# Performance work log

Measured on AMD Instinct MI355X. Metric: run time of the kernel, lower is better.

The kernel has to match this reference:

```python
import jax, jax.numpy as jnp
import numpy as np

HIDDEN = 2048
INTER = 8192
COMPRESSION = 128.9

def _n_ctrl(out_size, in_size):
    return max(16, int(out_size * in_size / COMPRESSION))

def _catmull_rom_grid(n_ctrl, n_samples):
    # static (numpy, float64) sampling grid over [0, n_ctrl-1] to avoid fp32 precision loss
    t = np.linspace(0.0, n_ctrl - 1.0, n_samples, dtype=np.float64)
    i = np.clip(np.floor(t).astype(np.int64), 0, n_ctrl - 2)
    f = (t - i).astype(np.float32)
    idx = np.stack([np.clip(i + k, 0, n_ctrl - 1) for k in (-1, 0, 1, 2)], axis=0)  # [4, N]
    return jnp.asarray(idx.astype(np.int32)), jnp.asarray(f)

def spline_reconstruct(control_points, out_size, in_size):
    """Cubic (Catmull-Rom, order-3) interpolation of 1D control points to a dense [out,in] weight."""
    n = out_size * in_size
    idx, f = _catmull_rom_grid(control_points.shape[0], n)
    p0, p1, p2, p3 = control_points[idx[0]], control_points[idx[1]], control_points[idx[2]], control_points[idx[3]]
    f2 = f * f
    f3 = f2 * f
    w = 0.5 * (2.0 * p1 + (p2 - p0) * f
               + (2.0 * p0 - 5.0 * p1 + 4.0 * p2 - p3) * f2
               + (3.0 * p1 - p0 - 3.0 * p2 + p3) * f3)
    return w.reshape(out_size, in_size)

def setup_inputs() -> dict:
    key = jax.random.key(0)
    k0, k1, k2, k3 = jax.random.split(key, 4)
    hidden_states = jax.random.normal(k0, (4, 2048, HIDDEN), dtype=jnp.float32)
    gate_cp = jax.random.normal(k1, (_n_ctrl(INTER, HIDDEN),), dtype=jnp.float32) * 0.02
    up_cp = jax.random.normal(k2, (_n_ctrl(INTER, HIDDEN),), dtype=jnp.float32) * 0.02
    down_cp = jax.random.normal(k3, (_n_ctrl(HIDDEN, INTER),), dtype=jnp.float32) * 0.02
    return {"hidden_states": hidden_states, "gate_cp": gate_cp, "up_cp": up_cp, "down_cp": down_cp}

def reference(hidden_states, gate_cp, up_cp, down_cp):
    gate_w = spline_reconstruct(gate_cp, INTER, HIDDEN)   # [I, H]
    up_w = spline_reconstruct(up_cp, INTER, HIDDEN)       # [I, H]
    down_w = spline_reconstruct(down_cp, HIDDEN, INTER)   # [H, I]
    gate = jnp.einsum('bsh,ih->bsi', hidden_states, gate_w)
    up = jnp.einsum('bsh,ih->bsi', hidden_states, up_w)
    inter = jax.nn.silu(gate) * up
    return jnp.einsum('bsi,hi->bsh', inter, down_w)
```

## Files before the change

### kernel.cpp

```cpp
#include <hip/hip_runtime.h>
#include <hip/hip_bf16.h>
#include <math.h>

using bf16 = __hip_bfloat16;
typedef __bf16 bf16x8 __attribute__((ext_vector_type(8)));
typedef float  f32x4  __attribute__((ext_vector_type(4)));

#define BK 64

__global__ void spline_recon8_kernel(const float* __restrict__ cp,
                                     bf16* __restrict__ w,
                                     int n8, int n_ctrl, double step) {
    int k8 = blockIdx.x * blockDim.x + threadIdx.x;
    if (k8 >= n8) return;
    long long kbase = (long long)k8 * 8;
    bf16x8 o;
#pragma unroll
    for (int u = 0; u < 8; ++u) {
        double t = (double)(kbase + u) * step;
        int i = (int)t;
        if (i > n_ctrl - 2) i = n_ctrl - 2;
        float f = (float)(t - (double)i);
        float p0 = cp[i > 0 ? i - 1 : 0];
        float p1 = cp[i];
        float p2 = cp[i + 1];
        float p3 = cp[(i + 2) <= (n_ctrl - 1) ? (i + 2) : (n_ctrl - 1)];
        float f2 = f * f;
        float f3 = f2 * f;
        float v = 0.5f * (2.0f * p1
                          + (p2 - p0) * f
                          + (2.0f * p0 - 5.0f * p1 + 4.0f * p2 - p3) * f2
                          + (3.0f * p1 - p0 - 3.0f * p2 + p3) * f3);
        o[u] = (__bf16)v;
    }
    *reinterpret_cast<bf16x8*>(w + kbase) = o;
}

__global__ void cvt_f32_bf16_8_kernel(const float4* __restrict__ x,
                                      bf16* __restrict__ y, int n8) {
    int k = blockIdx.x * blockDim.x + threadIdx.x;
    if (k >= n8) return;
    float4 a = x[2 * k];
    float4 b = x[2 * k + 1];
    bf16x8 o;
    o[0] = (__bf16)a.x; o[1] = (__bf16)a.y; o[2] = (__bf16)a.z; o[3] = (__bf16)a.w;
    o[4] = (__bf16)b.x; o[5] = (__bf16)b.y; o[6] = (__bf16)b.z; o[7] = (__bf16)b.w;
    *reinterpret_cast<bf16x8*>(y + (long long)k * 8) = o;
}

__device__ __forceinline__ void async_load16(const bf16* g, bf16* l) {
    __builtin_amdgcn_global_load_lds(
        (const __attribute__((address_space(1))) void*)g,
        (__attribute__((address_space(3))) void*)l,
        16, 0, 0);
}

__device__ __forceinline__ void raw_barrier() {
    asm volatile("" ::: "memory");
    __builtin_amdgcn_s_barrier();
    asm volatile("" ::: "memory");
}

#define WAIT_VM6() asm volatile("s_waitcnt vmcnt(6)" ::: "memory")
#define WAIT_VM0() asm volatile("s_waitcnt vmcnt(0)" ::: "memory")

__global__ __launch_bounds__(512, 2) void fused_gate_up_kernel(
    const bf16* __restrict__ A,
    const bf16* __restrict__ Bg,
    const bf16* __restrict__ Bu,
    bf16* __restrict__ C,
    int M, int N, int K) {
    __shared__ __align__(16) bf16 smem[2 * 3 * 128 * BK];
    bf16* As0  = smem;
    bf16* Bgs0 = smem + 8192;
    bf16* Bus0 = smem + 16384;
    bf16* As1  = smem + 24576;
    bf16* Bgs1 = smem + 32768;
    bf16* Bus1 = smem + 40960;

    const int tid  = threadIdx.x;
    const int lane = tid & 63;
    const int wave = tid >> 6;
    const int wq   = wave & 3;
    const int wm   = (wq >> 1) * 64;
    const int wn   = (wq & 1) * 64;
    const bool is_gate = wave < 4;

    const long long brow = (long long)blockIdx.y * 128;
    const long long bcol = (long long)blockIdx.x * 128;

    const int srow = tid >> 3;
    const int skb  = ((tid & 7) ^ (srow & 7)) * 8;
    const bf16* ga0 = A  + (brow + srow) * (long long)K + skb;
    const bf16* ga1 = A  + (brow + srow + 64) * (long long)K + skb;
    const bf16* gg0 = Bg + (bcol + srow) * (long long)K + skb;
    const bf16* gg1 = Bg + (bcol + srow + 64) * (long long)K + skb;
    const bf16* gu0 = Bu + (bcol + srow) * (long long)K + skb;
    const bf16* gu1 = Bu + (bcol + srow + 64) * (long long)K + skb;

    const int fm = wm + (lane & 15);
    const int fn = wn + (lane & 15);
    const int qk = lane >> 4;

    f32x4 acc[4][4] = {};

#define STAGE_F(dA, dG, dU, t)                                             \
    do {                                                                   \
        long long off = (long long)(t) * BK;                               \
        async_load16(ga0 + off, (dA) + tid * 8);                           \
        async_load16(ga1 + off, (dA) + 4096 + tid * 8);                    \
        async_load16(gg0 + off, (dG) + tid * 8);                           \
        async_load16(gg1 + off, (dG) + 4096 + tid * 8);                    \
        async_load16(gu0 + off, (dU) + tid * 8);                           \
        async_load16(gu1 + off, (dU) + 4096 + tid * 8);                    \
    } while (0)

#define COMPUTE_F(sA, sG, sU)                                              \
    do {                                                                   \
        const bf16* sB = is_gate ? (sG) : (sU);                            \
        _Pragma("unroll")                                                  \
        for (int h = 0; h < 2; ++h) {                                      \
            bf16x8 afr[4], bfr[4];                                         \
            const int hc = (h << 2) | qk;                                  \
            const int ccA = (hc ^ (fm & 7)) * 8;                           \
            const int ccB = (hc ^ (fn & 7)) * 8;                           \
            _Pragma("unroll")                                              \
            for (int i = 0; i < 4; ++i)                                    \
                afr[i] = *reinterpret_cast<const bf16x8*>(                 \
                    &(sA)[(fm + i * 16) * BK + ccA]);                      \
            _Pragma("unroll")                                              \
            for (int j = 0; j < 4; ++j)                                    \
                bfr[j] = *reinterpret_cast<const bf16x8*>(                 \
                    &sB[(fn + j * 16) * BK + ccB]);                        \
            _Pragma("unroll")                                              \
            for (int i = 0; i < 4; ++i)                                    \
                _Pragma("unroll")                                          \
                for (int j = 0; j < 4; ++j)                                \
                    acc[i][j] = __builtin_amdgcn_mfma_f32_16x16x32_bf16(   \
                        afr[i], bfr[j], acc[i][j], 0, 0, 0);               \
        }                                                                  \
    } while (0)

    const int nt = K / BK;

    STAGE_F(As0, Bgs0, Bus0, 0);
    STAGE_F(As1, Bgs1, Bus1, 1);
    WAIT_VM6();
    raw_barrier();

    for (int t = 0; t + 2 < nt; t += 2) {
        COMPUTE_F(As0, Bgs0, Bus0);
        raw_barrier();
        STAGE_F(As0, Bgs0, Bus0, t + 2);
        WAIT_VM6();
        raw_barrier();
        COMPUTE_F(As1, Bgs1, Bus1);
        raw_barrier();
        STAGE_F(As1, Bgs1, Bus1, t + 3);
        WAIT_VM6();
        raw_barrier();
    }
    COMPUTE_F(As0, Bgs0, Bus0);
    WAIT_VM0();
    raw_barrier();
    COMPUTE_F(As1, Bgs1, Bus1);
#undef STAGE_F
#undef COMPUTE_F

    bf16* Epi = smem;
    if (is_gate) {
#pragma unroll
        for (int i = 0; i < 4; ++i)
#pragma unroll
            for (int j = 0; j < 4; ++j)
#pragma unroll
                for (int r = 0; r < 4; ++r) {
                    int row = wm + i * 16 + (lane >> 4) * 4 + r;
                    int col = wn + j * 16 + (lane & 15);
                    float v = acc[i][j][r];
                    float s = v / (1.0f + expf(-v));
                    Epi[row * 128 + col] = __float2bfloat16(s);
                }
    }
    __syncthreads();
    if (!is_gate) {
#pragma unroll
        for (int i = 0; i < 4; ++i)
#pragma unroll
            for (int j = 0; j < 4; ++j)
#pragma unroll
                for (int r = 0; r < 4; ++r) {
                    int row = wm + i * 16 + (lane >> 4) * 4 + r;
                    int col = wn + j * 16 + (lane & 15);
                    float s = __bfloat162float(Epi[row * 128 + col]);
                    float v = s * acc[i][j][r];
                    C[(brow + row) * (long long)N + bcol + col] = __float2bfloat16(v);
                }
    }
}

__global__ __launch_bounds__(512, 2) void gemm_down6_kernel(
    const bf16* __restrict__ A,
    const bf16* __restrict__ B,
    float* __restrict__ C,
    int M, int N, int K) {
    __shared__ __align__(16) bf16 smem[2 * 3 * 128 * BK];
    bf16* As0 = smem;
    bf16* Bs0 = smem + 128 * BK;
    bf16* As1 = smem + 3 * 128 * BK;
    bf16* Bs1 = smem + 4 * 128 * BK;

    const int tid  = threadIdx.x;
    const int lane = tid & 63;
    const int wave = tid >> 6;
    const int wm   = (wave >> 2) * 64;
    const int wn   = (wave & 3) * 64;

    const int b = blockIdx.x;
    const long long brow = (long long)((b & 7) * 8 + (b >> 6)) * 128;
    const long long bcol = (long long)((b >> 3) & 7) * 256;

    const int srow = tid >> 3;
    const int skb  = ((tid & 7) ^ (srow & 7)) * 8;
    const bf16* ga0 = A + (brow + srow) * (long long)K + skb;
    const bf16* ga1 = A + (brow + srow + 64) * (long long)K + skb;
    const bf16* gb0 = B + (bcol + srow) * (long long)K + skb;
    const bf16* gb1 = B + (bcol + srow + 64) * (long long)K + skb;
    const bf16* gb2 = B + (bcol + srow + 128) * (long long)K + skb;
    const bf16* gb3 = B + (bcol + srow + 192) * (long long)K + skb;

    const int fm = wm + (lane & 15);
    const int fn = wn + (lane & 15);
    const int qk = lane >> 4;

    f32x4 acc[4][4] = {};

#define STAGE_DOWN(dA, dB, t)                                              \
    do {                                                                   \
        long long off = (long long)(t) * BK;                               \
        async_load16(ga0 + off, (dA) + tid * 8);                           \
        async_load16(ga1 + off, (dA) + 4096 + tid * 8);                    \
        async_load16(gb0 + off, (dB) + tid * 8);                           \
        async_load16(gb1 + off, (dB) + 4096 + tid * 8);                    \
        async_load16(gb2 + off, (dB) + 8192 + tid * 8);                    \
        async_load16(gb3 + off, (dB) + 12288 + tid * 8);                   \
    } while (0)

#define COMPUTE_DOWN(sA, sB)                                               \
    do {                                                                   \
        _Pragma("unroll")                                                  \
        for (int h = 0; h < 2; ++h) {                                      \
            bf16x8 afr[4], bfr[4];                                         \
            const int hc = (h << 2) | qk;                                  \
            const int ccA = (hc ^ (fm & 7)) * 8;                           \
            const int ccB = (hc ^ (fn & 7)) * 8;                           \
            _Pragma("unroll")                                              \
            for (int i = 0; i < 4; ++i)                                    \
                afr[i] = *reinterpret_cast<const bf16x8*>(                 \
                    &(sA)[(fm + i * 16) * BK + ccA]);                      \
            _Pragma("unroll")                                              \
            for (int j = 0; j < 4; ++j)                                    \
                bfr[j] = *reinterpret_cast<const bf16x8*>(                 \
                    &(sB)[(fn + j * 16) * BK + ccB]);                      \
            _Pragma("unroll")                                              \
            for (int i = 0; i < 4; ++i)                                    \
                _Pragma("unroll")                                          \
                for (int j = 0; j < 4; ++j)                                \
                    acc[i][j] = __builtin_amdgcn_mfma_f32_16x16x32_bf16(   \
                        afr[i], bfr[j], acc[i][j], 0, 0, 0);               \
        }                                                                  \
    } while (0)

    const int nt = K / BK;

    STAGE_DOWN(As0, Bs0, 0);
    STAGE_DOWN(As1, Bs1, 1);
    WAIT_VM6();
    raw_barrier();

    for (int t = 0; t + 2 < nt; t += 2) {
        COMPUTE_DOWN(As0, Bs0);
        raw_barrier();
        STAGE_DOWN(As0, Bs0, t + 2);
        WAIT_VM6();
        raw_barrier();
        COMPUTE_DOWN(As1, Bs1);
        raw_barrier();
        STAGE_DOWN(As1, Bs1, t + 3);
        WAIT_VM6();
        raw_barrier();
    }
    COMPUTE_DOWN(As0, Bs0);
    WAIT_VM0();
    raw_barrier();
    COMPUTE_DOWN(As1, Bs1);
#undef STAGE_DOWN
#undef COMPUTE_DOWN

#pragma unroll
    for (int i = 0; i < 4; ++i)
#pragma unroll
        for (int j = 0; j < 4; ++j)
#pragma unroll
            for (int r = 0; r < 4; ++r) {
                long long row = brow + wm + i * 16 + qk * 4 + r;
                long long col = bcol + wn + j * 16 + (lane & 15);
                C[row * N + col] = acc[i][j][r];
            }
}

extern "C" void kernel_launch(void* const* d_in, const int* in_sizes, int n_in,
                              void* d_out, int out_size, void* d_ws, size_t ws_size,
                              hipStream_t stream) {
    const float* hs  = (const float*)d_in[0];
    const float* gcp = (const float*)d_in[1];
    const float* ucp = (const float*)d_in[2];
    const float* dcp = (const float*)d_in[3];

    const int M = 8192;
    const int H = 2048;
    const int I = 8192;
    const int NW = H * I;
    const int n_ctrl_g = in_sizes[1];
    const int n_ctrl_u = in_sizes[2];
    const int n_ctrl_d = in_sizes[3];

    bf16* Xb    = (bf16*)d_ws;
    bf16* Wg    = Xb + (size_t)M * H;
    bf16* Wu    = Wg + (size_t)NW;
    bf16* Wd    = Wu + (size_t)NW;
    bf16* inter = Wd + (size_t)NW;

    const int nX8 = (M * H) / 8;
    cvt_f32_bf16_8_kernel<<<(nX8 + 255) / 256, 256, 0, stream>>>(
        (const float4*)hs, Xb, nX8);

    double step_g = (double)(n_ctrl_g - 1) / (double)(NW - 1);
    double step_u = (double)(n_ctrl_u - 1) / (double)(NW - 1);
    double step_d = (double)(n_ctrl_d - 1) / (double)(NW - 1);
    const int n8 = NW / 8;
    spline_recon8_kernel<<<(n8 + 255) / 256, 256, 0, stream>>>(gcp, Wg, n8, n_ctrl_g, step_g);
    spline_recon8_kernel<<<(n8 + 255) / 256, 256, 0, stream>>>(ucp, Wu, n8, n_ctrl_u, step_u);
    spline_recon8_kernel<<<(n8 + 255) / 256, 256, 0, stream>>>(dcp, Wd, n8, n_ctrl_d, step_d);

    fused_gate_up_kernel<<<dim3(I / 128, M / 128), 512, 0, stream>>>(
        Xb, Wg, Wu, inter, M, I, H);

    gemm_down6_kernel<<<512, 512, 0, stream>>>(
        inter, Wd, (float*)d_out, M, H, I);
}
```

Measured before the change: 952.4 us.

## Enlarge GEMM tiles to 256 rows and compute gate and up per wave

The fused gate/up kernel now uses a 256x128 tile in which every wave computes both the gate and up accumulators. The SiLU*up epilogue happens in registers, so the LDS round-trip and the extra syncthreads go away and the A tile gets more reuse. The down GEMM moves to 256x256 tiles with 8x4 accumulator fragments per wave, halving the grid to 256 blocks. Each wave now holds twice the accumulators and LDS use grows to 128KB per block, so register spills or lower occupancy are possible despite the launch bound of 2.

```diff
diff --git a/kernel.cpp b/kernel.cpp
--- a/kernel.cpp
+++ b/kernel.cpp
@@ -61,38 +61,38 @@
     asm volatile("" ::: "memory");
 }
 
-#define WAIT_VM6() asm volatile("s_waitcnt vmcnt(6)" ::: "memory")
-#define WAIT_VM0() asm volatile("s_waitcnt vmcnt(0)" ::: "memory")
-
-__global__ __launch_bounds__(512, 2) void fused_gate_up_kernel(
+#define WAIT_VM8()  asm volatile("s_waitcnt vmcnt(8)" ::: "memory")
+#define WAIT_VM0()  asm volatile("s_waitcnt vmcnt(0)" ::: "memory")
+
+__global__ __launch_bounds__(512, 2) void fused_gate_up2_kernel(
     const bf16* __restrict__ A,
     const bf16* __restrict__ Bg,
     const bf16* __restrict__ Bu,
     bf16* __restrict__ C,
     int M, int N, int K) {
-    __shared__ __align__(16) bf16 smem[2 * 3 * 128 * BK];
+    __shared__ __align__(16) bf16 smem[2 * 2 * 256 * BK];
     bf16* As0  = smem;
-    bf16* Bgs0 = smem + 8192;
-    bf16* Bus0 = smem + 16384;
-    bf16* As1  = smem + 24576;
-    bf16* Bgs1 = smem + 32768;
-    bf16* Bus1 = smem + 40960;
+    bf16* Bgs0 = smem + 16384;
+    bf16* Bus0 = smem + 24576;
+    bf16* As1  = smem + 32768;
+    bf16* Bgs1 = smem + 49152;
+    bf16* Bus1 = smem + 57344;
 
     const int tid  = threadIdx.x;
     const int lane = tid & 63;
     const int wave = tid >> 6;
-    const int wq   = wave & 3;
-    const int wm   = (wq >> 1) * 64;
-    const int wn   = (wq & 1) * 64;
-    const bool is_gate = wave < 4;
-
-    const long long brow = (long long)blockIdx.y * 128;
+    const int wm   = (wave >> 1) * 64;
+    const int wn   = (wave & 1) * 64;
+
+    const long long brow = (long long)blockIdx.y * 256;
     const long long bcol = (long long)blockIdx.x * 128;
 
     const int srow = tid >> 3;
     const int skb  = ((tid & 7) ^ (srow & 7)) * 8;
     const bf16* ga0 = A  + (brow + srow) * (long long)K + skb;
     const bf16* ga1 = A  + (brow + srow + 64) * (long long)K + skb;
+    const bf16* ga2 = A  + (brow + srow + 128) * (long long)K + skb;
+    const bf16* ga3 = A  + (brow + srow + 192) * (long long)K + skb;
     const bf16* gg0 = Bg + (bcol + srow) * (long long)K + skb;
     const bf16* gg1 = Bg + (bcol + srow + 64) * (long long)K + skb;
     const bf16* gu0 = Bu + (bcol + srow) * (long long)K + skb;
@@ -102,13 +102,16 @@
     const int fn = wn + (lane & 15);
     const int qk = lane >> 4;
 
-    f32x4 acc[4][4] = {};
+    f32x4 acc_g[4][4] = {};
+    f32x4 acc_u[4][4] = {};
 
 #define STAGE_F(dA, dG, dU, t)                                             \
     do {                                                                   \
         long long off = (long long)(t) * BK;                               \
         async_load16(ga0 + off, (dA) + tid * 8);                           \
         async_load16(ga1 + off, (dA) + 4096 + tid * 8);                    \
+        async_load16(ga2 + off, (dA) + 8192 + tid * 8);                    \
+        async_load16(ga3 + off, (dA) + 12288 + tid * 8);                   \
         async_load16(gg0 + off, (dG) + tid * 8);                           \
         async_load16(gg1 + off, (dG) + 4096 + tid * 8);                    \
         async_load16(gu0 + off, (dU) + tid * 8);                           \
@@ -117,10 +120,9 @@
 
 #define COMPUTE_F(sA, sG, sU)                                              \
     do {                                                                   \
-        const bf16* sB = is_gate ? (sG) : (sU);                            \
         _Pragma("unroll")                                                  \
         for (int h = 0; h < 2; ++h) {                                      \
-            bf16x8 afr[4], bfr[4];                                         \
+            bf16x8 afr[4], bgr[4], bur[4];                                 \
             const int hc = (h << 2) | qk;                                  \
             const int ccA = (hc ^ (fm & 7)) * 8;                           \
             const int ccB = (hc ^ (fn & 7)) * 8;                           \
@@ -129,15 +131,21 @@
                 afr[i] = *reinterpret_cast<const bf16x8*>(                 \
                     &(sA)[(fm + i * 16) * BK + ccA]);                      \
             _Pragma("unroll")                                              \
-            for (int j = 0; j < 4; ++j)                                    \
-                bfr[j] = *reinterpret_cast<const bf16x8*>(                 \
-                    &sB[(fn + j * 16) * BK + ccB]);                        \
+            for (int j = 0; j < 4; ++j) {                                  \
+                bgr[j] = *reinterpret_cast<const bf16x8*>(                 \
+                    &(sG)[(fn + j * 16) * BK + ccB]);                      \
+                bur[j] = *reinterpret_cast<const bf16x8*>(                 \
+                    &(sU)[(fn + j * 16) * BK + ccB]);                      \
+            }                                                              \
             _Pragma("unroll")                                              \
             for (int i = 0; i < 4; ++i)                                    \
                 _Pragma("unroll")                                          \
-                for (int j = 0; j < 4; ++j)                                \
-                    acc[i][j] = __builtin_amdgcn_mfma_f32_16x16x32_bf16(   \
-                        afr[i], bfr[j], acc[i][j], 0, 0, 0);               \
+                for (int j = 0; j < 4; ++j) {                              \
+                    acc_g[i][j] = __builtin_amdgcn_mfma_f32_16x16x32_bf16( \
+                        afr[i], bgr[j], acc_g[i][j], 0, 0, 0);             \
+                    acc_u[i][j] = __builtin_amdgcn_mfma_f32_16x16x32_bf16( \
+                        afr[i], bur[j], acc_u[i][j], 0, 0, 0);             \
+                }                                                          \
         }                                                                  \
     } while (0)
 
@@ -145,19 +153,19 @@
 
     STAGE_F(As0, Bgs0, Bus0, 0);
     STAGE_F(As1, Bgs1, Bus1, 1);
-    WAIT_VM6();
+    WAIT_VM8();
     raw_barrier();
 
     for (int t = 0; t + 2 < nt; t += 2) {
         COMPUTE_F(As0, Bgs0, Bus0);
         raw_barrier();
         STAGE_F(As0, Bgs0, Bus0, t + 2);
-        WAIT_VM6();
+        WAIT_VM8();
         raw_barrier();
         COMPUTE_F(As1, Bgs1, Bus1);
         raw_barrier();
         STAGE_F(As1, Bgs1, Bus1, t + 3);
-        WAIT_VM6();
+        WAIT_VM8();
         raw_barrier();
     }
     COMPUTE_F(As0, Bgs0, Bus0);
@@ -167,95 +175,74 @@
 #undef STAGE_F
 #undef COMPUTE_F
 
-    bf16* Epi = smem;
-    if (is_gate) {
-#pragma unroll
-        for (int i = 0; i < 4; ++i)
-#pragma unroll
-            for (int j = 0; j < 4; ++j)
-#pragma unroll
-                for (int r = 0; r < 4; ++r) {
-                    int row = wm + i * 16 + (lane >> 4) * 4 + r;
-                    int col = wn + j * 16 + (lane & 15);
-                    float v = acc[i][j][r];
-                    float s = v / (1.0f + expf(-v));
-                    Epi[row * 128 + col] = __float2bfloat16(s);
-                }
-    }
-    __syncthreads();
-    if (!is_gate) {
-#pragma unroll
-        for (int i = 0; i < 4; ++i)
-#pragma unroll
-            for (int j = 0; j < 4; ++j)
-#pragma unroll
-                for (int r = 0; r < 4; ++r) {
-                    int row = wm + i * 16 + (lane >> 4) * 4 + r;
-                    int col = wn + j * 16 + (lane & 15);
-                    float s = __bfloat162float(Epi[row * 128 + col]);
-                    float v = s * acc[i][j][r];
-                    C[(brow + row) * (long long)N + bcol + col] = __float2bfloat16(v);
-                }
-    }
-}
-
-__global__ __launch_bounds__(512, 2) void gemm_down6_kernel(
+#pragma unroll
+    for (int i = 0; i < 4; ++i)
+#pragma unroll
+        for (int j = 0; j < 4; ++j)
+#pragma unroll
+            for (int r = 0; r < 4; ++r) {
+                long long row = brow + wm + i * 16 + qk * 4 + r;
+                long long col = bcol + wn + j * 16 + (lane & 15);
+                float g = acc_g[i][j][r];
+                float u = acc_u[i][j][r];
+                float s = g / (1.0f + expf(-g));
+                C[row * (long long)N + col] = __float2bfloat16(s * u);
+            }
+}
+
+__global__ __launch_bounds__(512, 2) void gemm_down8_kernel(
     const bf16* __restrict__ A,
     const bf16* __restrict__ B,
     float* __restrict__ C,
     int M, int N, int K) {
-    __shared__ __align__(16) bf16 smem[2 * 3 * 128 * BK];
+    __shared__ __align__(16) bf16 smem[2 * 2 * 256 * BK];
     bf16* As0 = smem;
-    bf16* Bs0 = smem + 128 * BK;
-    bf16* As1 = smem + 3 * 128 * BK;
-    bf16* Bs1 = smem + 4 * 128 * BK;
+    bf16* Bs0 = smem + 16384;
+    bf16* As1 = smem + 32768;
+    bf16* Bs1 = smem + 49152;
 
     const int tid  = threadIdx.x;
     const int lane = tid & 63;
     const int wave = tid >> 6;
-    const int wm   = (wave >> 2) * 64;
+    const int wm   = (wave >> 2) * 128;
     const int wn   = (wave & 3) * 64;
 
     const int b = blockIdx.x;
-    const long long brow = (long long)((b & 7) * 8 + (b >> 6)) * 128;
+    const long long brow = (long long)((b & 7) * 4 + (b >> 6)) * 256;
     const long long bcol = (long long)((b >> 3) & 7) * 256;
 
     const int srow = tid >> 3;
     const int skb  = ((tid & 7) ^ (srow & 7)) * 8;
-    const bf16* ga0 = A + (brow + srow) * (long long)K + skb;
-    const bf16* ga1 = A + (brow + srow + 64) * (long long)K + skb;
-    const bf16* gb0 = B + (bcol + srow) * (long long)K + skb;
-    const bf16* gb1 = B + (bcol + srow + 64) * (long long)K + skb;
-    const bf16* gb2 = B + (bcol + srow + 128) * (long long)K + skb;
-    const bf16* gb3 = B + (bcol + srow + 192) * (long long)K + skb;
+    const bf16* gaR = A + (brow + srow) * (long long)K + skb;
+    const bf16* gbR = B + (bcol + srow) * (long long)K + skb;
+    const long long rstep = 64LL * K;
 
     const int fm = wm + (lane & 15);
     const int fn = wn + (lane & 15);
     const int qk = lane >> 4;
 
-    f32x4 acc[4][4] = {};
+    f32x4 acc[8][4] = {};
 
 #define STAGE_DOWN(dA, dB, t)                                              \
     do {                                                                   \
         long long off = (long long)(t) * BK;                               \
-        async_load16(ga0 + off, (dA) + tid * 8);                           \
-        async_load16(ga1 + off, (dA) + 4096 + tid * 8);                    \
-        async_load16(gb0 + off, (dB) + tid * 8);                           \
-        async_load16(gb1 + off, (dB) + 4096 + tid * 8);                    \
-        async_load16(gb2 + off, (dB) + 8192 + tid * 8);                    \
-        async_load16(gb3 + off, (dB) + 12288 + tid * 8);                   \
+        _Pragma("unroll")                                                  \
+        for (int r = 0; r < 4; ++r) {                                      \
+            async_load16(gaR + r * rstep + off, (dA) + r * 4096 + tid * 8);\
+            async_load16(gbR + r * rstep + off, (dB) + r * 4096 + tid * 8);\
+        }                                                                  \
     } while (0)
 
 #define COMPUTE_DOWN(sA, sB)                                               \
     do {                                                                   \
         _Pragma("unroll")                                                  \
         for (int h = 0; h < 2; ++h) {                                      \
-            bf16x8 afr[4], bfr[4];                                         \
+            bf16x8 afr[8], bfr[4];                                         \
             const int hc = (h << 2) | qk;                                  \
             const int ccA = (hc ^ (fm & 7)) * 8;                           \
             const int ccB = (hc ^ (fn & 7)) * 8;                           \
             _Pragma("unroll")                                              \
-            for (int i = 0; i < 4; ++i)                                    \
+            for (int i = 0; i < 8; ++i)                                    \
                 afr[i] = *reinterpret_cast<const bf16x8*>(                 \
                     &(sA)[(fm + i * 16) * BK + ccA]);                      \
             _Pragma("unroll")                                              \
@@ -263,7 +250,7 @@
                 bfr[j] = *reinterpret_cast<const bf16x8*>(                 \
                     &(sB)[(fn + j * 16) * BK + ccB]);                      \
             _Pragma("unroll")                                              \
-            for (int i = 0; i < 4; ++i)                                    \
+            for (int i = 0; i < 8; ++i)                                    \
                 _Pragma("unroll")                                          \
                 for (int j = 0; j < 4; ++j)                                \
                     acc[i][j] = __builtin_amdgcn_mfma_f32_16x16x32_bf16(   \
@@ -275,19 +262,19 @@
 
     STAGE_DOWN(As0, Bs0, 0);
     STAGE_DOWN(As1, Bs1, 1);
-    WAIT_VM6();
+    WAIT_VM8();
     raw_barrier();
 
     for (int t = 0; t + 2 < nt; t += 2) {
         COMPUTE_DOWN(As0, Bs0);
         raw_barrier();
         STAGE_DOWN(As0, Bs0, t + 2);
-        WAIT_VM6();
+        WAIT_VM8();
         raw_barrier();
         COMPUTE_DOWN(As1, Bs1);
         raw_barrier();
         STAGE_DOWN(As1, Bs1, t + 3);
-        WAIT_VM6();
+        WAIT_VM8();
         raw_barrier();
     }
     COMPUTE_DOWN(As0, Bs0);
@@ -298,7 +285,7 @@
 #undef COMPUTE_DOWN
 
 #pragma unroll
-    for (int i = 0; i < 4; ++i)
+    for (int i = 0; i < 8; ++i)
 #pragma unroll
         for (int j = 0; j < 4; ++j)
 #pragma unroll
@@ -343,9 +330,9 @@
     spline_recon8_kernel<<<(n8 + 255) / 256, 256, 0, stream>>>(ucp, Wu, n8, n_ctrl_u, step_u);
     spline_recon8_kernel<<<(n8 + 255) / 256, 256, 0, stream>>>(dcp, Wd, n8, n_ctrl_d, step_d);
 
-    fused_gate_up_kernel<<<dim3(I / 128, M / 128), 512, 0, stream>>>(
+    fused_gate_up2_kernel<<<dim3(I / 128, M / 256), 512, 0, stream>>>(
         Xb, Wg, Wu, inter, M, I, H);
 
-    gemm_down6_kernel<<<512, 512, 0, stream>>>(
+    gemm_down8_kernel<<<256, 512, 0, stream>>>(
         inter, Wd, (float*)d_out, M, H, I);
 }
```

After: 1.090 ms. 14.4% more time.
